# Kernel optimization log

Measured on AMD Instinct MI355X. Metric: run time of the kernel, lower is better.

Reference implementation:

```python
import jax, jax.numpy as jnp
import numpy as np

B, S, D, H = 4, 2048, 512, 8
DH = D // H


def setup_inputs() -> dict:
    key = jax.random.key(0)
    ks = jax.random.split(key, 6)
    embeddings = jax.random.normal(ks[0], (B, S, D), dtype=jnp.float32)
    token_masks = jax.random.randint(ks[1], (B, S), 0, 2, dtype=jnp.int32)
    # keras 'random_normal' initializer: stddev 0.05
    Wq = 0.05 * jax.random.normal(ks[2], (D, D), dtype=jnp.float32)
    Wk = 0.05 * jax.random.normal(ks[3], (D, D), dtype=jnp.float32)
    Wv = 0.05 * jax.random.normal(ks[4], (D, D), dtype=jnp.float32)
    Wo = 0.05 * jax.random.normal(ks[5], (D, D), dtype=jnp.float32)
    return {"embeddings": embeddings, "token_masks": token_masks,
            "Wq": Wq, "Wk": Wk, "Wv": Wv, "Wo": Wo}


def reference(embeddings, token_masks, Wq, Wk, Wv, Wo):
    b, s, d = embeddings.shape
    h, dh = H, d // H
    # QKV projections -> (b, h, s, dh)
    def split_heads(x):
        return x.reshape(b, s, h, dh).transpose(0, 2, 1, 3)
    Q = split_heads(embeddings @ Wq)
    K = split_heads(embeddings @ Wk)
    V = split_heads(embeddings @ Wv)
    scores = jnp.einsum('bhqd,bhkd->bhqk', Q, K) / jnp.sqrt(jnp.float32(dh))
    # causal (lower-triangular) mask combined with padding mask on both q and k
    causal = jnp.tril(jnp.ones((s, s), dtype=jnp.float32))
    tm = token_masks.astype(jnp.float32)
    attn_mask = causal[None, None, :, :] * tm[:, None, None, :] * tm[:, None, :, None]
    scores = jnp.where(attn_mask > 0, scores, jnp.float32(-1e30))
    weights = jax.nn.softmax(scores, axis=-1)  # dropout omitted (inference/eval mode)
    context = jnp.einsum('bhqk,bhkd->bhqd', weights, V)
    context = context.transpose(0, 2, 1, 3).reshape(b, s, d)
    return context @ Wo
```

## Files before the change

kernel.cpp:

```cpp
#include <hip/hip_runtime.h>
#include <hip/hip_bf16.h>
#include <stdint.h>

#define BATCH 4
#define SEQ 2048
#define DMODEL 512
#define NHEAD 8
#define HD 64

#define C1 0.18033688f
#define BIAS2 -23.0831207f

using f32x4 = __attribute__((ext_vector_type(4))) float;
using bfrag = __attribute__((ext_vector_type(8))) short;

__device__ __forceinline__ short f2bf(float f) {
  uint32_t x = __builtin_bit_cast(uint32_t, f);
  uint32_t r = (x + 0x7fffu + ((x >> 16) & 1u)) >> 16;
  return (short)r;
}
__device__ __forceinline__ short f2bf_fast(float f) {
  return (short)((__builtin_bit_cast(uint32_t, f) + 0x8000u) >> 16);
}
__device__ __forceinline__ float bf2f(short s) {
  return __builtin_bit_cast(float, ((uint32_t)(uint16_t)s) << 16);
}
__device__ __forceinline__ void gl_lds16(const void* g, void* l) {
  __builtin_amdgcn_global_load_lds(
      (const __attribute__((address_space(1))) void*)g,
      (__attribute__((address_space(3))) void*)l, 16, 0, 0);
}
__device__ __forceinline__ bool sniff_f32(const void* p, int tid) {
  const uint32_t* xw = (const uint32_t*)p;
  const int lane = tid & 63;
  const uint32_t w1 = xw[lane], w2 = xw[64 + lane];
  bool bad = (((w1 >> 7) & 0xffu) >= 0xB0u) | (((w1 >> 23) & 0xffu) >= 0xB0u) |
             (((w2 >> 7) & 0xffu) >= 0xB0u) | (((w2 >> 23) & 0xffu) >= 0xB0u);
  return __ballot(bad) != 0ull;
}

__global__ __launch_bounds__(256) void prep(const void* __restrict__ X,
                                            const void* __restrict__ w0,
                                            const void* __restrict__ w1,
                                            const void* __restrict__ w2,
                                            const void* __restrict__ w3,
                                            short* __restrict__ Xb,
                                            short* __restrict__ wtAll,
                                            float* __restrict__ mv) {
  const int blk = blockIdx.x, tid = threadIdx.x;
  if (blk < 2048) {
    const bool isf32 = sniff_f32(X, tid);
    const int i = (blk * 256 + tid) * 8;
    if (isf32) {
      const float* f = (const float*)X;
      short r[8];
#pragma unroll
      for (int j = 0; j < 8; ++j) r[j] = f2bf(f[i + j]);
      *(bfrag*)&Xb[i] = *(bfrag*)r;
    } else {
      *(bfrag*)&Xb[i] = *(const bfrag*)&((const short*)X)[i];
    }
  } else if (blk < 3072) {
    __shared__ short t[32][33];
    const int idx = blk - 2048;
    const int z = idx >> 8, rem = idx & 255;
    const void* in = (z == 0) ? w0 : (z == 1) ? w1 : (z == 2) ? w2 : w3;
    short* out = wtAll + (size_t)z * DMODEL * DMODEL;
    const int tx = tid & 31, ty = tid >> 5;
    const bool isf32 = sniff_f32(in, tid);
    const int n0 = (rem & 15) * 32, k0 = (rem >> 4) * 32;
#pragma unroll
    for (int i = ty; i < 32; i += 8) {
      const int idx2 = (k0 + i) * DMODEL + n0 + tx;
      t[i][tx] = isf32 ? f2bf(((const float*)in)[idx2]) : ((const short*)in)[idx2];
    }
    __syncthreads();
#pragma unroll
    for (int i = ty; i < 32; i += 8) out[(n0 + i) * DMODEL + k0 + tx] = t[tx][i];
  } else {
#pragma unroll
    for (int j = 0; j < 8; ++j) mv[tid * 8 + j] = 0.f;
  }
}

__global__ __launch_bounds__(256) void gemm_qkv(const short* __restrict__ X,
                                                const short* __restrict__ WtAll,
                                                short* __restrict__ Qo,
                                                short* __restrict__ Ko,
                                                short* __restrict__ Vo,
                                                float* __restrict__ mv) {
  __shared__ __align__(16) short As[128 * 32];
  __shared__ __align__(16) short Bs[128 * 32];
  const int which = blockIdx.z;
  const short* Wt = WtAll + which * DMODEL * DMODEL;
  const int m0 = blockIdx.y * 128, n0 = blockIdx.x * 128;
  const int tid = threadIdx.x, lane = tid & 63, wave = tid >> 6;
  const int l15 = lane & 15, quad = lane >> 4;
  const int wm = wave >> 1, wn = wave & 1;
  const int lrow = lane >> 2, lcol = (lane & 3) * 8;
  f32x4 acc[4][4] = {};
  for (int kc = 0; kc < DMODEL; kc += 32) {
#pragma unroll
    for (int i = 0; i < 2; ++i) {
      const int r0 = (wave * 2 + i) * 16;
      gl_lds16(&X[(size_t)(m0 + r0 + lrow) * DMODEL + kc + lcol], &As[r0 * 32]);
      gl_lds16(&Wt[(size_t)(n0 + r0 + lrow) * DMODEL + kc + lcol], &Bs[r0 * 32]);
    }
    __syncthreads();
    bfrag a[4], b[4];
#pragma unroll
    for (int t = 0; t < 4; ++t) {
      a[t] = *(const bfrag*)&As[(wm * 64 + t * 16 + l15) * 32 + quad * 8];
      b[t] = *(const bfrag*)&Bs[(wn * 64 + t * 16 + l15) * 32 + quad * 8];
    }
#pragma unroll
    for (int tm = 0; tm < 4; ++tm)
#pragma unroll
      for (int tn = 0; tn < 4; ++tn)
        acc[tm][tn] = __builtin_amdgcn_mfma_f32_16x16x32_bf16(a[tm], b[tn], acc[tm][tn], 0, 0, 0);
    __syncthreads();
  }
  short* O = (which == 0) ? Qo : (which == 1) ? Ko : Vo;
#pragma unroll
  for (int tn = 0; tn < 4; ++tn) {
    const int col = n0 + wn * 64 + tn * 16 + l15;
    const int h = col >> 6, d = col & 63;
#pragma unroll
    for (int tm = 0; tm < 4; ++tm) {
#pragma unroll
      for (int r = 0; r < 4; ++r) {
        const int row = m0 + wm * 64 + tm * 16 + quad * 4 + r;
        const int b = row >> 11, s = row & 2047;
        O[((b * NHEAD + h) * SEQ + s) * HD + d] = f2bf(acc[tm][tn][r]);
      }
    }
  }
  if (which == 2) {
    const int b = (m0 + wm * 64) >> 11;
#pragma unroll
    for (int tn = 0; tn < 4; ++tn) {
      float s = 0.f;
#pragma unroll
      for (int tm = 0; tm < 4; ++tm)
#pragma unroll
        for (int r = 0; r < 4; ++r) s += acc[tm][tn][r];
      s += __shfl_xor(s, 16);
      s += __shfl_xor(s, 32);
      if (quad == 0) {
        const int col = n0 + wn * 64 + tn * 16 + l15;
        const int h = col >> 6, d = col & 63;
        atomicAdd(&mv[(b * NHEAD + h) * 64 + d], s);
      }
    }
  }
}

__global__ __launch_bounds__(256) void gemm_out(const short* __restrict__ X,
                                                const short* __restrict__ Wt,
                                                float* __restrict__ O) {
  __shared__ __align__(16) short As[128 * 32];
  __shared__ __align__(16) short Bs[128 * 32];
  const int m0 = blockIdx.y * 128, n0 = blockIdx.x * 128;
  const int tid = threadIdx.x, lane = tid & 63, wave = tid >> 6;
  const int l15 = lane & 15, quad = lane >> 4;
  const int wm = wave >> 1, wn = wave & 1;
  const int lrow = lane >> 2, lcol = (lane & 3) * 8;
  f32x4 acc[4][4] = {};
  for (int kc = 0; kc < DMODEL; kc += 32) {
#pragma unroll
    for (int i = 0; i < 2; ++i) {
      const int r0 = (wave * 2 + i) * 16;
      gl_lds16(&X[(size_t)(m0 + r0 + lrow) * DMODEL + kc + lcol], &As[r0 * 32]);
      gl_lds16(&Wt[(size_t)(n0 + r0 + lrow) * DMODEL + kc + lcol], &Bs[r0 * 32]);
    }
    __syncthreads();
    bfrag a[4], b[4];
#pragma unroll
    for (int t = 0; t < 4; ++t) {
      a[t] = *(const bfrag*)&As[(wm * 64 + t * 16 + l15) * 32 + quad * 8];
      b[t] = *(const bfrag*)&Bs[(wn * 64 + t * 16 + l15) * 32 + quad * 8];
    }
#pragma unroll
    for (int tm = 0; tm < 4; ++tm)
#pragma unroll
      for (int tn = 0; tn < 4; ++tn)
        acc[tm][tn] = __builtin_amdgcn_mfma_f32_16x16x32_bf16(a[tm], b[tn], acc[tm][tn], 0, 0, 0);
    __syncthreads();
  }
#pragma unroll
  for (int tm = 0; tm < 4; ++tm)
#pragma unroll
    for (int tn = 0; tn < 4; ++tn) {
      const int col = n0 + wn * 64 + tn * 16 + l15;
#pragma unroll
      for (int r = 0; r < 4; ++r) {
        const int row = m0 + wm * 64 + tm * 16 + quad * 4 + r;
        O[(size_t)row * DMODEL + col] = acc[tm][tn][r];
      }
    }
}

__global__ __launch_bounds__(256, 4) void attn(const short* __restrict__ Q,
                                               const short* __restrict__ K,
                                               const short* __restrict__ V,
                                               const int* __restrict__ tmask,
                                               const float* __restrict__ meanV,
                                               short* __restrict__ ctx) {
  __shared__ __align__(16) short Ks[64 * 72];
  __shared__ __align__(16) short Vts[64 * 64];
  __shared__ __align__(16) short Ps[4 * 16 * 64];
  __shared__ int tmq[64];
  __shared__ int tmk[64];
  const int m2 = blockIdx.x >> 3, a3 = blockIdx.x & 7;
  const int j2 = blockIdx.y >> 3, b3 = blockIdx.y & 7;
  const int quart = (m2 + j2) & 3;
  const int qi = quart * 8 + ((quart & 1) ? (7 - a3) : a3);
  const int bh = j2 * 8 + b3;
  const int b = bh >> 3, h = bh & 7;
  const int q0 = qi * 64;
  const int tid = threadIdx.x, lane = tid & 63, wave = tid >> 6;
  const int l15 = lane & 15, quad = lane >> 4;
  const size_t base = (size_t)bh * SEQ * HD;

  bfrag qa0 = *(const bfrag*)&Q[base + (size_t)(q0 + wave * 16 + l15) * HD + quad * 8];
  bfrag qa1 = *(const bfrag*)&Q[base + (size_t)(q0 + wave * 16 + l15) * HD + 32 + quad * 8];
  if (tid < 64) tmq[tid] = tmask[b * SEQ + q0 + tid];

  f32x4 accO[4] = {};
  float lrow[4] = {0.f, 0.f, 0.f, 0.f};

  const int rp = tid >> 3, sgp = tid & 7;
  bfrag kA, kB, vA, vB;
  int tmreg = 0;

  auto prefetch = [&](int kc) {
    const size_t o0 = base + (size_t)(kc + 2 * rp) * HD + sgp * 8;
    kA = *(const bfrag*)&K[o0];
    kB = *(const bfrag*)&K[o0 + HD];
    vA = *(const bfrag*)&V[o0];
    vB = *(const bfrag*)&V[o0 + HD];
    if (tid < 64) tmreg = tmask[b * SEQ + kc + tid];
  };
  auto store_lds = [&]() {
    *(bfrag*)&Ks[(2 * rp) * 72 + sgp * 8] = kA;
    *(bfrag*)&Ks[(2 * rp + 1) * 72 + sgp * 8] = kB;
    const int g = ((rp >> 2) ^ ((sgp & 1) << 2) ^ (sgp >> 1)) & 7;
    const int kpos = (2 * rp) & 7;
#pragma unroll
    for (int j = 0; j < 8; ++j) {
      const uint32_t w = (uint32_t)(uint16_t)vA[j] | ((uint32_t)(uint16_t)vB[j] << 16);
      *(uint32_t*)&Vts[(sgp * 8 + j) * 64 + g * 8 + kpos] = w;
    }
    if (tid < 64) tmk[tid] = tmreg;
  };
  auto compute = [&](bool diag) {
    f32x4 sacc[4] = {};
#pragma unroll
    for (int t = 0; t < 4; ++t) {
      bfrag b0 = *(const bfrag*)&Ks[(t * 16 + l15) * 72 + quad * 8];
      sacc[t] = __builtin_amdgcn_mfma_f32_16x16x32_bf16(qa0, b0, sacc[t], 0, 0, 0);
    }
#pragma unroll
    for (int t = 0; t < 4; ++t) {
      bfrag b1 = *(const bfrag*)&Ks[(t * 16 + l15) * 72 + 32 + quad * 8];
      sacc[t] = __builtin_amdgcn_mfma_f32_16x16x32_bf16(qa1, b1, sacc[t], 0, 0, 0);
    }
    float badd[4];
#pragma unroll
    for (int t = 0; t < 4; ++t) badd[t] = tmk[t * 16 + l15] ? BIAS2 : -1e30f;
#pragma unroll
    for (int r = 0; r < 4; ++r) {
      const int m = quad * 4 + r;
#pragma unroll
      for (int t = 0; t < 4; ++t) {
        float p = exp2f(fmaf(sacc[t][r], C1, badd[t]));
        if (diag && (t * 16 + l15 > wave * 16 + m)) p = 0.f;
        lrow[r] += p;
        const int g = ((t * 2 + (l15 >> 3)) ^ (m & 7) ^ ((m >> 3) << 1)) & 7;
        Ps[wave * 1024 + m * 64 + g * 8 + (l15 & 7)] = f2bf_fast(p);
      }
    }
#pragma unroll
    for (int ks = 0; ks < 2; ++ks) {
#pragma unroll
      for (int t = 0; t < 4; ++t) {
        const int gp = ((ks * 4 + quad) ^ (l15 & 7) ^ ((l15 >> 3) << 1)) & 7;
        bfrag pa = *(const bfrag*)&Ps[wave * 1024 + l15 * 64 + gp * 8];
        const int d = t * 16 + l15;
        const int gv = ((ks * 4 + quad) ^ ((l15 >> 3) << 2) ^ t) & 7;
        bfrag vb = *(const bfrag*)&Vts[d * 64 + gv * 8];
        accO[t] = __builtin_amdgcn_mfma_f32_16x16x32_bf16(pa, vb, accO[t], 0, 0, 0);
      }
    }
  };

  prefetch(0);
  for (int kc = 0; kc <= q0; kc += 64) {
    __syncthreads();
    store_lds();
    __syncthreads();
    if (kc < q0) prefetch(kc + 64);
    compute(kc == q0);
  }

#pragma unroll
  for (int r = 0; r < 4; ++r) {
    float l = lrow[r];
    l += __shfl_xor(l, 1);
    l += __shfl_xor(l, 2);
    l += __shfl_xor(l, 4);
    l += __shfl_xor(l, 8);
    lrow[r] = 1.f / l;
  }
  const int qrow_loc = wave * 16 + quad * 4;
#pragma unroll
  for (int t = 0; t < 4; ++t) {
    const int d = t * 16 + l15;
    const float mvd = meanV[bh * 64 + d] * (1.f / 2048.f);
#pragma unroll
    for (int r = 0; r < 4; ++r) {
      const int row = qrow_loc + r;
      float val = accO[t][r] * lrow[r];
      if (tmq[row] == 0) val = mvd;
      ctx[((size_t)(b * SEQ + q0 + row)) * DMODEL + h * HD + d] = f2bf(val);
    }
  }
}

extern "C" void kernel_launch(void* const* d_in, const int* in_sizes, int n_in,
                              void* d_out, int out_size, void* d_ws, size_t ws_size,
                              hipStream_t stream) {
  const void* X = d_in[0];
  const int* tmask = (const int*)d_in[1];
  const void* Wq = d_in[2];
  const void* Wk = d_in[3];
  const void* Wv = d_in[4];
  const void* Wo = d_in[5];
  float* out = (float*)d_out;
  char* ws = (char*)d_ws;

  const size_t WELEM = (size_t)DMODEL * DMODEL;
  const size_t TELEM = (size_t)BATCH * NHEAD * SEQ * HD;

  float* mv = (float*)(ws + 4096);
  short* wt = (short*)(ws + 4096 + 8192);
  short* Xb = (short*)(ws + 4096 + 8192 + 2097152);
  short* Qb = Xb + TELEM;
  short* Kb = Qb + TELEM;
  short* Vb = Kb + TELEM;
  short* Cb = Vb + TELEM;

  prep<<<3073, 256, 0, stream>>>(X, Wq, Wk, Wv, Wo, Xb, wt, mv);
  gemm_qkv<<<dim3(4, 64, 3), 256, 0, stream>>>(Xb, wt, Qb, Kb, Vb, mv);
  attn<<<dim3(32, 32), 256, 0, stream>>>(Qb, Kb, Vb, tmask, mv, Cb);
  gemm_out<<<dim3(4, 64), 256, 0, stream>>>(Cb, wt + 3 * WELEM, out);
}
```

Before: 172.8 us.

## Keep attention probabilities in registers via transposed QK and permlane swaps

```diff
diff --git a/kernel.cpp b/kernel.cpp
--- a/kernel.cpp
+++ b/kernel.cpp
@@ -13,14 +13,12 @@
 
 using f32x4 = __attribute__((ext_vector_type(4))) float;
 using bfrag = __attribute__((ext_vector_type(8))) short;
+using u32x4 = __attribute__((ext_vector_type(4))) unsigned int;
 
 __device__ __forceinline__ short f2bf(float f) {
   uint32_t x = __builtin_bit_cast(uint32_t, f);
   uint32_t r = (x + 0x7fffu + ((x >> 16) & 1u)) >> 16;
   return (short)r;
-}
-__device__ __forceinline__ short f2bf_fast(float f) {
-  return (short)((__builtin_bit_cast(uint32_t, f) + 0x8000u) >> 16);
 }
 __device__ __forceinline__ float bf2f(short s) {
   return __builtin_bit_cast(float, ((uint32_t)(uint16_t)s) << 16);
@@ -37,6 +35,17 @@
   bool bad = (((w1 >> 7) & 0xffu) >= 0xB0u) | (((w1 >> 23) & 0xffu) >= 0xB0u) |
              (((w2 >> 7) & 0xffu) >= 0xB0u) | (((w2 >> 23) & 0xffu) >= 0xB0u);
   return __ballot(bad) != 0ull;
+}
+__device__ __forceinline__ uint32_t cvtpk(float lo, float hi) {
+  uint32_t r;
+  asm("v_cvt_pk_bf16_f32 %0, %1, %2" : "=v"(r) : "v"(lo), "v"(hi));
+  return r;
+}
+__device__ __forceinline__ void pl32swap(uint32_t& a, uint32_t& b) {
+  asm("v_permlane32_swap_b32 %0, %1" : "+v"(a), "+v"(b));
+}
+__device__ __forceinline__ void pl16swap(uint32_t& a, uint32_t& b) {
+  asm("v_permlane16_swap_b32 %0, %1" : "+v"(a), "+v"(b));
 }
 
 __global__ __launch_bounds__(256) void prep(const void* __restrict__ X,
@@ -208,9 +217,7 @@
                                                short* __restrict__ ctx) {
   __shared__ __align__(16) short Ks[64 * 72];
   __shared__ __align__(16) short Vts[64 * 64];
-  __shared__ __align__(16) short Ps[4 * 16 * 64];
   __shared__ int tmq[64];
-  __shared__ int tmk[64];
   const int m2 = blockIdx.x >> 3, a3 = blockIdx.x & 7;
   const int j2 = blockIdx.y >> 3, b3 = blockIdx.y & 7;
   const int quart = (m2 + j2) & 3;
@@ -227,11 +234,12 @@
   if (tid < 64) tmq[tid] = tmask[b * SEQ + q0 + tid];
 
   f32x4 accO[4] = {};
-  float lrow[4] = {0.f, 0.f, 0.f, 0.f};
+  float lq = 0.f;
+  const int qrow_w = wave * 16 + l15;
 
   const int rp = tid >> 3, sgp = tid & 7;
   bfrag kA, kB, vA, vB;
-  int tmreg = 0;
+  uint64_t km_next = 0;
 
   auto prefetch = [&](int kc) {
     const size_t o0 = base + (size_t)(kc + 2 * rp) * HD + sgp * 8;
@@ -239,7 +247,8 @@
     kB = *(const bfrag*)&K[o0 + HD];
     vA = *(const bfrag*)&V[o0];
     vB = *(const bfrag*)&V[o0 + HD];
-    if (tid < 64) tmreg = tmask[b * SEQ + kc + tid];
+    const int mt = tmask[b * SEQ + kc + lane];
+    km_next = __ballot(mt != 0);
   };
   auto store_lds = [&]() {
     *(bfrag*)&Ks[(2 * rp) * 72 + sgp * 8] = kA;
@@ -251,45 +260,47 @@
       const uint32_t w = (uint32_t)(uint16_t)vA[j] | ((uint32_t)(uint16_t)vB[j] << 16);
       *(uint32_t*)&Vts[(sgp * 8 + j) * 64 + g * 8 + kpos] = w;
     }
-    if (tid < 64) tmk[tid] = tmreg;
   };
-  auto compute = [&](bool diag) {
+  auto compute = [&](bool diag, uint64_t km) {
     f32x4 sacc[4] = {};
 #pragma unroll
     for (int t = 0; t < 4; ++t) {
-      bfrag b0 = *(const bfrag*)&Ks[(t * 16 + l15) * 72 + quad * 8];
-      sacc[t] = __builtin_amdgcn_mfma_f32_16x16x32_bf16(qa0, b0, sacc[t], 0, 0, 0);
-    }
-#pragma unroll
-    for (int t = 0; t < 4; ++t) {
-      bfrag b1 = *(const bfrag*)&Ks[(t * 16 + l15) * 72 + 32 + quad * 8];
-      sacc[t] = __builtin_amdgcn_mfma_f32_16x16x32_bf16(qa1, b1, sacc[t], 0, 0, 0);
-    }
-    float badd[4];
-#pragma unroll
-    for (int t = 0; t < 4; ++t) badd[t] = tmk[t * 16 + l15] ? BIAS2 : -1e30f;
-#pragma unroll
-    for (int r = 0; r < 4; ++r) {
-      const int m = quad * 4 + r;
+      bfrag k0 = *(const bfrag*)&Ks[(t * 16 + l15) * 72 + quad * 8];
+      sacc[t] = __builtin_amdgcn_mfma_f32_16x16x32_bf16(k0, qa0, sacc[t], 0, 0, 0);
+      bfrag k1 = *(const bfrag*)&Ks[(t * 16 + l15) * 72 + 32 + quad * 8];
+      sacc[t] = __builtin_amdgcn_mfma_f32_16x16x32_bf16(k1, qa1, sacc[t], 0, 0, 0);
+    }
+#pragma unroll
+    for (int ks = 0; ks < 2; ++ks) {
+      uint32_t w[4];
+#pragma unroll
+      for (int hh = 0; hh < 2; ++hh) {
+        const int t = 2 * ks + hh;
+        float pr[4];
+#pragma unroll
+        for (int r = 0; r < 4; ++r) {
+          const int k = t * 16 + quad * 4 + r;
+          const float badd = ((km >> k) & 1ull) ? BIAS2 : -1e30f;
+          float pv = exp2f(fmaf(sacc[t][r], C1, badd));
+          if (diag && (k > qrow_w)) pv = 0.f;
+          lq += pv;
+          pr[r] = pv;
+        }
+        w[2 * hh] = cvtpk(pr[0], pr[1]);
+        w[2 * hh + 1] = cvtpk(pr[2], pr[3]);
+      }
+      pl32swap(w[0], w[2]);
+      pl16swap(w[0], w[2]);
+      pl32swap(w[1], w[3]);
+      pl16swap(w[1], w[3]);
+      u32x4 pw = {w[0], w[1], w[2], w[3]};
+      bfrag paf = __builtin_bit_cast(bfrag, pw);
 #pragma unroll
       for (int t = 0; t < 4; ++t) {
-        float p = exp2f(fmaf(sacc[t][r], C1, badd[t]));
-        if (diag && (t * 16 + l15 > wave * 16 + m)) p = 0.f;
-        lrow[r] += p;
-        const int g = ((t * 2 + (l15 >> 3)) ^ (m & 7) ^ ((m >> 3) << 1)) & 7;
-        Ps[wave * 1024 + m * 64 + g * 8 + (l15 & 7)] = f2bf_fast(p);
-      }
-    }
-#pragma unroll
-    for (int ks = 0; ks < 2; ++ks) {
-#pragma unroll
-      for (int t = 0; t < 4; ++t) {
-        const int gp = ((ks * 4 + quad) ^ (l15 & 7) ^ ((l15 >> 3) << 1)) & 7;
-        bfrag pa = *(const bfrag*)&Ps[wave * 1024 + l15 * 64 + gp * 8];
         const int d = t * 16 + l15;
         const int gv = ((ks * 4 + quad) ^ ((l15 >> 3) << 2) ^ t) & 7;
         bfrag vb = *(const bfrag*)&Vts[d * 64 + gv * 8];
-        accO[t] = __builtin_amdgcn_mfma_f32_16x16x32_bf16(pa, vb, accO[t], 0, 0, 0);
+        accO[t] = __builtin_amdgcn_mfma_f32_16x16x32_bf16(paf, vb, accO[t], 0, 0, 0);
       }
     }
   };
@@ -298,20 +309,18 @@
   for (int kc = 0; kc <= q0; kc += 64) {
     __syncthreads();
     store_lds();
+    const uint64_t km = km_next;
     __syncthreads();
     if (kc < q0) prefetch(kc + 64);
-    compute(kc == q0);
-  }
-
-#pragma unroll
-  for (int r = 0; r < 4; ++r) {
-    float l = lrow[r];
-    l += __shfl_xor(l, 1);
-    l += __shfl_xor(l, 2);
-    l += __shfl_xor(l, 4);
-    l += __shfl_xor(l, 8);
-    lrow[r] = 1.f / l;
-  }
+    compute(kc == q0, km);
+  }
+
+  lq += __shfl_xor(lq, 16);
+  lq += __shfl_xor(lq, 32);
+  float linv[4];
+#pragma unroll
+  for (int r = 0; r < 4; ++r) linv[r] = 1.f / __shfl(lq, quad * 4 + r, 64);
+
   const int qrow_loc = wave * 16 + quad * 4;
 #pragma unroll
   for (int t = 0; t < 4; ++t) {
@@ -320,7 +329,7 @@
 #pragma unroll
     for (int r = 0; r < 4; ++r) {
       const int row = qrow_loc + r;
-      float val = accO[t][r] * lrow[r];
+      float val = accO[t][r] * linv[r];
       if (tmq[row] == 0) val = mvd;
       ctx[((size_t)(b * SEQ + q0 + row)) * DMODEL + h * HD + d] = f2bf(val);
     }
```

Result: slower. 178.7 us (+3.4%).

## Load K fragments directly into registers and ballot the key mask

Applied to the files above, without the earlier changes.

```diff
diff --git a/kernel.cpp b/kernel.cpp
--- a/kernel.cpp
+++ b/kernel.cpp
@@ -206,11 +206,9 @@
                                                const int* __restrict__ tmask,
                                                const float* __restrict__ meanV,
                                                short* __restrict__ ctx) {
-  __shared__ __align__(16) short Ks[64 * 72];
   __shared__ __align__(16) short Vts[64 * 64];
   __shared__ __align__(16) short Ps[4 * 16 * 64];
   __shared__ int tmq[64];
-  __shared__ int tmk[64];
   const int m2 = blockIdx.x >> 3, a3 = blockIdx.x & 7;
   const int j2 = blockIdx.y >> 3, b3 = blockIdx.y & 7;
   const int quart = (m2 + j2) & 3;
@@ -230,20 +228,26 @@
   float lrow[4] = {0.f, 0.f, 0.f, 0.f};
 
   const int rp = tid >> 3, sgp = tid & 7;
-  bfrag kA, kB, vA, vB;
-  int tmreg = 0;
-
-  auto prefetch = [&](int kc) {
+  bfrag vA, vB;
+  bfrag kf0[4], kf1[4];
+  uint64_t km_next = 0;
+
+  auto prefetch_v = [&](int kc) {
     const size_t o0 = base + (size_t)(kc + 2 * rp) * HD + sgp * 8;
-    kA = *(const bfrag*)&K[o0];
-    kB = *(const bfrag*)&K[o0 + HD];
     vA = *(const bfrag*)&V[o0];
     vB = *(const bfrag*)&V[o0 + HD];
-    if (tid < 64) tmreg = tmask[b * SEQ + kc + tid];
+    const int mt = tmask[b * SEQ + kc + lane];
+    km_next = __ballot(mt != 0);
+  };
+  auto loadK = [&](int kc) {
+#pragma unroll
+    for (int t = 0; t < 4; ++t) {
+      const size_t ro = base + (size_t)(kc + t * 16 + l15) * HD + quad * 8;
+      kf0[t] = *(const bfrag*)&K[ro];
+      kf1[t] = *(const bfrag*)&K[ro + 32];
+    }
   };
   auto store_lds = [&]() {
-    *(bfrag*)&Ks[(2 * rp) * 72 + sgp * 8] = kA;
-    *(bfrag*)&Ks[(2 * rp + 1) * 72 + sgp * 8] = kB;
     const int g = ((rp >> 2) ^ ((sgp & 1) << 2) ^ (sgp >> 1)) & 7;
     const int kpos = (2 * rp) & 7;
 #pragma unroll
@@ -251,23 +255,19 @@
       const uint32_t w = (uint32_t)(uint16_t)vA[j] | ((uint32_t)(uint16_t)vB[j] << 16);
       *(uint32_t*)&Vts[(sgp * 8 + j) * 64 + g * 8 + kpos] = w;
     }
-    if (tid < 64) tmk[tid] = tmreg;
   };
-  auto compute = [&](bool diag) {
+  auto compute = [&](bool diag, uint64_t km, int kc) {
     f32x4 sacc[4] = {};
 #pragma unroll
     for (int t = 0; t < 4; ++t) {
-      bfrag b0 = *(const bfrag*)&Ks[(t * 16 + l15) * 72 + quad * 8];
-      sacc[t] = __builtin_amdgcn_mfma_f32_16x16x32_bf16(qa0, b0, sacc[t], 0, 0, 0);
-    }
-#pragma unroll
-    for (int t = 0; t < 4; ++t) {
-      bfrag b1 = *(const bfrag*)&Ks[(t * 16 + l15) * 72 + 32 + quad * 8];
-      sacc[t] = __builtin_amdgcn_mfma_f32_16x16x32_bf16(qa1, b1, sacc[t], 0, 0, 0);
-    }
+      sacc[t] = __builtin_amdgcn_mfma_f32_16x16x32_bf16(qa0, kf0[t], sacc[t], 0, 0, 0);
+      sacc[t] = __builtin_amdgcn_mfma_f32_16x16x32_bf16(qa1, kf1[t], sacc[t], 0, 0, 0);
+    }
+    if (kc < q0) loadK(kc + 64);
     float badd[4];
 #pragma unroll
-    for (int t = 0; t < 4; ++t) badd[t] = tmk[t * 16 + l15] ? BIAS2 : -1e30f;
+    for (int t = 0; t < 4; ++t)
+      badd[t] = ((km >> (t * 16 + l15)) & 1ull) ? BIAS2 : -1e30f;
 #pragma unroll
     for (int r = 0; r < 4; ++r) {
       const int m = quad * 4 + r;
@@ -294,13 +294,15 @@
     }
   };
 
-  prefetch(0);
+  prefetch_v(0);
+  loadK(0);
   for (int kc = 0; kc <= q0; kc += 64) {
     __syncthreads();
     store_lds();
-    __syncthreads();
-    if (kc < q0) prefetch(kc + 64);
-    compute(kc == q0);
+    const uint64_t km = km_next;
+    __syncthreads();
+    if (kc < q0) prefetch_v(kc + 64);
+    compute(kc == q0, km, kc);
   }
 
 #pragma unroll
```

New measurement: 230.6 us. +33.5%, slower.

## Balance causal attention work by split-K pairing of query tiles with combine kernel

Applied to the files above, without the earlier changes.

```diff
diff --git a/kernel.cpp b/kernel.cpp
--- a/kernel.cpp
+++ b/kernel.cpp
@@ -205,126 +205,182 @@
                                                const short* __restrict__ V,
                                                const int* __restrict__ tmask,
                                                const float* __restrict__ meanV,
-                                               short* __restrict__ ctx) {
+                                               short* __restrict__ ctx,
+                                               float* __restrict__ Pn0,
+                                               float* __restrict__ Pl0,
+                                               float* __restrict__ Pn1,
+                                               float* __restrict__ Pl1) {
   __shared__ __align__(16) short Ks[64 * 72];
   __shared__ __align__(16) short Vts[64 * 64];
   __shared__ __align__(16) short Ps[4 * 16 * 64];
-  __shared__ int tmq[64];
-  __shared__ int tmk[64];
-  const int m2 = blockIdx.x >> 3, a3 = blockIdx.x & 7;
-  const int j2 = blockIdx.y >> 3, b3 = blockIdx.y & 7;
-  const int quart = (m2 + j2) & 3;
-  const int qi = quart * 8 + ((quart & 1) ? (7 - a3) : a3);
-  const int bh = j2 * 8 + b3;
+  const int bh = blockIdx.x, j = blockIdx.y;
   const int b = bh >> 3, h = bh & 7;
-  const int q0 = qi * 64;
   const int tid = threadIdx.x, lane = tid & 63, wave = tid >> 6;
   const int l15 = lane & 15, quad = lane >> 4;
+  const int rp = tid >> 3, sgp = tid & 7;
   const size_t base = (size_t)bh * SEQ * HD;
 
-  bfrag qa0 = *(const bfrag*)&Q[base + (size_t)(q0 + wave * 16 + l15) * HD + quad * 8];
-  bfrag qa1 = *(const bfrag*)&Q[base + (size_t)(q0 + wave * 16 + l15) * HD + 32 + quad * 8];
-  if (tid < 64) tmq[tid] = tmask[b * SEQ + q0 + tid];
-
-  f32x4 accO[4] = {};
-  float lrow[4] = {0.f, 0.f, 0.f, 0.f};
-
-  const int rp = tid >> 3, sgp = tid & 7;
-  bfrag kA, kB, vA, vB;
-  int tmreg = 0;
-
-  auto prefetch = [&](int kc) {
-    const size_t o0 = base + (size_t)(kc + 2 * rp) * HD + sgp * 8;
-    kA = *(const bfrag*)&K[o0];
-    kB = *(const bfrag*)&K[o0 + HD];
-    vA = *(const bfrag*)&V[o0];
-    vB = *(const bfrag*)&V[o0 + HD];
-    if (tid < 64) tmreg = tmask[b * SEQ + kc + tid];
+  auto run_phase = [&](int q0, int kc0, int nch, bool dg, bool direct,
+                       float* pn, float* pl) {
+    bfrag qa0 = *(const bfrag*)&Q[base + (size_t)(q0 + wave * 16 + l15) * HD + quad * 8];
+    bfrag qa1 = *(const bfrag*)&Q[base + (size_t)(q0 + wave * 16 + l15) * HD + 32 + quad * 8];
+    f32x4 accO[4] = {};
+    float lrow[4] = {0.f, 0.f, 0.f, 0.f};
+    bfrag kA, kB, vA, vB;
+    uint64_t km_next = 0;
+
+    auto prefetch = [&](int kc) {
+      const size_t o0 = base + (size_t)(kc + 2 * rp) * HD + sgp * 8;
+      kA = *(const bfrag*)&K[o0];
+      kB = *(const bfrag*)&K[o0 + HD];
+      vA = *(const bfrag*)&V[o0];
+      vB = *(const bfrag*)&V[o0 + HD];
+      km_next = __ballot(tmask[b * SEQ + kc + lane] != 0);
+    };
+    auto store_lds = [&]() {
+      *(bfrag*)&Ks[(2 * rp) * 72 + sgp * 8] = kA;
+      *(bfrag*)&Ks[(2 * rp + 1) * 72 + sgp * 8] = kB;
+      const int g = ((rp >> 2) ^ ((sgp & 1) << 2) ^ (sgp >> 1)) & 7;
+      const int kpos = (2 * rp) & 7;
+#pragma unroll
+      for (int jj = 0; jj < 8; ++jj) {
+        const uint32_t w = (uint32_t)(uint16_t)vA[jj] | ((uint32_t)(uint16_t)vB[jj] << 16);
+        *(uint32_t*)&Vts[(sgp * 8 + jj) * 64 + g * 8 + kpos] = w;
+      }
+    };
+    auto compute = [&](bool diag, uint64_t km) {
+      f32x4 sacc[4] = {};
+#pragma unroll
+      for (int t = 0; t < 4; ++t) {
+        bfrag b0 = *(const bfrag*)&Ks[(t * 16 + l15) * 72 + quad * 8];
+        sacc[t] = __builtin_amdgcn_mfma_f32_16x16x32_bf16(qa0, b0, sacc[t], 0, 0, 0);
+      }
+#pragma unroll
+      for (int t = 0; t < 4; ++t) {
+        bfrag b1 = *(const bfrag*)&Ks[(t * 16 + l15) * 72 + 32 + quad * 8];
+        sacc[t] = __builtin_amdgcn_mfma_f32_16x16x32_bf16(qa1, b1, sacc[t], 0, 0, 0);
+      }
+      float badd[4];
+#pragma unroll
+      for (int t = 0; t < 4; ++t)
+        badd[t] = ((km >> (t * 16 + l15)) & 1ull) ? BIAS2 : -1e30f;
+#pragma unroll
+      for (int r = 0; r < 4; ++r) {
+        const int m = quad * 4 + r;
+#pragma unroll
+        for (int t = 0; t < 4; ++t) {
+          float p = exp2f(fmaf(sacc[t][r], C1, badd[t]));
+          if (diag && (t * 16 + l15 > wave * 16 + m)) p = 0.f;
+          lrow[r] += p;
+          const int g = ((t * 2 + (l15 >> 3)) ^ (m & 7) ^ ((m >> 3) << 1)) & 7;
+          Ps[wave * 1024 + m * 64 + g * 8 + (l15 & 7)] = f2bf_fast(p);
+        }
+      }
+#pragma unroll
+      for (int ks = 0; ks < 2; ++ks) {
+#pragma unroll
+        for (int t = 0; t < 4; ++t) {
+          const int gp = ((ks * 4 + quad) ^ (l15 & 7) ^ ((l15 >> 3) << 1)) & 7;
+          bfrag pa = *(const bfrag*)&Ps[wave * 1024 + l15 * 64 + gp * 8];
+          const int d = t * 16 + l15;
+          const int gv = ((ks * 4 + quad) ^ ((l15 >> 3) << 2) ^ t) & 7;
+          bfrag vb = *(const bfrag*)&Vts[d * 64 + gv * 8];
+          accO[t] = __builtin_amdgcn_mfma_f32_16x16x32_bf16(pa, vb, accO[t], 0, 0, 0);
+        }
+      }
+    };
+
+    prefetch(kc0);
+    for (int c = 0; c < nch; ++c) {
+      const int kc = kc0 + c * 64;
+      __syncthreads();
+      store_lds();
+      const uint64_t km = km_next;
+      __syncthreads();
+      if (c + 1 < nch) prefetch(kc + 64);
+      compute(dg && (c == nch - 1), km);
+    }
+
+#pragma unroll
+    for (int r = 0; r < 4; ++r) {
+      float l = lrow[r];
+      l += __shfl_xor(l, 1);
+      l += __shfl_xor(l, 2);
+      l += __shfl_xor(l, 4);
+      l += __shfl_xor(l, 8);
+      lrow[r] = l;
+    }
+    const int qrow_loc = wave * 16 + quad * 4;
+    if (direct) {
+      const uint64_t qm = __ballot(tmask[b * SEQ + q0 + lane] != 0);
+      float inv[4];
+#pragma unroll
+      for (int r = 0; r < 4; ++r) inv[r] = 1.f / lrow[r];
+#pragma unroll
+      for (int t = 0; t < 4; ++t) {
+        const int d = t * 16 + l15;
+        const float mvd = meanV[bh * 64 + d] * (1.f / 2048.f);
+#pragma unroll
+        for (int r = 0; r < 4; ++r) {
+          const int row = qrow_loc + r;
+          float val = accO[t][r] * inv[r];
+          if (!((qm >> row) & 1ull)) val = mvd;
+          ctx[((size_t)(b * SEQ + q0 + row)) * DMODEL + h * HD + d] = f2bf(val);
+        }
+      }
+    } else {
+#pragma unroll
+      for (int t = 0; t < 4; ++t)
+#pragma unroll
+        for (int r = 0; r < 4; ++r)
+          pn[(qrow_loc + r) * 64 + t * 16 + l15] = accO[t][r];
+      if (l15 == 0) {
+#pragma unroll
+        for (int r = 0; r < 4; ++r) pl[qrow_loc + r] = lrow[r];
+      }
+    }
   };
-  auto store_lds = [&]() {
-    *(bfrag*)&Ks[(2 * rp) * 72 + sgp * 8] = kA;
-    *(bfrag*)&Ks[(2 * rp + 1) * 72 + sgp * 8] = kB;
-    const int g = ((rp >> 2) ^ ((sgp & 1) << 2) ^ (sgp >> 1)) & 7;
-    const int kpos = (2 * rp) & 7;
-#pragma unroll
-    for (int j = 0; j < 8; ++j) {
-      const uint32_t w = (uint32_t)(uint16_t)vA[j] | ((uint32_t)(uint16_t)vB[j] << 16);
-      *(uint32_t*)&Vts[(sgp * 8 + j) * 64 + g * 8 + kpos] = w;
-    }
-    if (tid < 64) tmk[tid] = tmreg;
-  };
-  auto compute = [&](bool diag) {
-    f32x4 sacc[4] = {};
-#pragma unroll
-    for (int t = 0; t < 4; ++t) {
-      bfrag b0 = *(const bfrag*)&Ks[(t * 16 + l15) * 72 + quad * 8];
-      sacc[t] = __builtin_amdgcn_mfma_f32_16x16x32_bf16(qa0, b0, sacc[t], 0, 0, 0);
-    }
-#pragma unroll
-    for (int t = 0; t < 4; ++t) {
-      bfrag b1 = *(const bfrag*)&Ks[(t * 16 + l15) * 72 + 32 + quad * 8];
-      sacc[t] = __builtin_amdgcn_mfma_f32_16x16x32_bf16(qa1, b1, sacc[t], 0, 0, 0);
-    }
-    float badd[4];
-#pragma unroll
-    for (int t = 0; t < 4; ++t) badd[t] = tmk[t * 16 + l15] ? BIAS2 : -1e30f;
-#pragma unroll
-    for (int r = 0; r < 4; ++r) {
-      const int m = quad * 4 + r;
-#pragma unroll
-      for (int t = 0; t < 4; ++t) {
-        float p = exp2f(fmaf(sacc[t][r], C1, badd[t]));
-        if (diag && (t * 16 + l15 > wave * 16 + m)) p = 0.f;
-        lrow[r] += p;
-        const int g = ((t * 2 + (l15 >> 3)) ^ (m & 7) ^ ((m >> 3) << 1)) & 7;
-        Ps[wave * 1024 + m * 64 + g * 8 + (l15 & 7)] = f2bf_fast(p);
-      }
-    }
-#pragma unroll
-    for (int ks = 0; ks < 2; ++ks) {
-#pragma unroll
-      for (int t = 0; t < 4; ++t) {
-        const int gp = ((ks * 4 + quad) ^ (l15 & 7) ^ ((l15 >> 3) << 1)) & 7;
-        bfrag pa = *(const bfrag*)&Ps[wave * 1024 + l15 * 64 + gp * 8];
-        const int d = t * 16 + l15;
-        const int gv = ((ks * 4 + quad) ^ ((l15 >> 3) << 2) ^ t) & 7;
-        bfrag vb = *(const bfrag*)&Vts[d * 64 + gv * 8];
-        accO[t] = __builtin_amdgcn_mfma_f32_16x16x32_bf16(pa, vb, accO[t], 0, 0, 0);
-      }
-    }
-  };
-
-  prefetch(0);
-  for (int kc = 0; kc <= q0; kc += 64) {
-    __syncthreads();
-    store_lds();
-    __syncthreads();
-    if (kc < q0) prefetch(kc + 64);
-    compute(kc == q0);
-  }
-
-#pragma unroll
-  for (int r = 0; r < 4; ++r) {
-    float l = lrow[r];
-    l += __shfl_xor(l, 1);
-    l += __shfl_xor(l, 2);
-    l += __shfl_xor(l, 4);
-    l += __shfl_xor(l, 8);
-    lrow[r] = 1.f / l;
-  }
-  const int qrow_loc = wave * 16 + quad * 4;
-#pragma unroll
-  for (int t = 0; t < 4; ++t) {
-    const int d = t * 16 + l15;
-    const float mvd = meanV[bh * 64 + d] * (1.f / 2048.f);
-#pragma unroll
-    for (int r = 0; r < 4; ++r) {
-      const int row = qrow_loc + r;
-      float val = accO[t][r] * lrow[r];
-      if (tmq[row] == 0) val = mvd;
-      ctx[((size_t)(b * SEQ + q0 + row)) * DMODEL + h * HD + d] = f2bf(val);
-    }
-  }
+
+  if (j < 16) {
+    run_phase(64 * j, 0, j + 1, true, true, nullptr, nullptr);
+    const int tl = 15 - j;
+    run_phase(64 * (31 - j), 1024, 16 - j, true, false,
+              Pn1 + (size_t)(bh * 16 + tl) * 4096, Pl1 + (bh * 16 + tl) * 64);
+  } else {
+    run_phase(64 * j, 0, 16, false, false,
+              Pn0 + (size_t)(bh * 16 + (j - 16)) * 4096,
+              Pl0 + (bh * 16 + (j - 16)) * 64);
+  }
+}
+
+__global__ __launch_bounds__(256) void combine(const float* __restrict__ Pn0,
+                                               const float* __restrict__ Pl0,
+                                               const float* __restrict__ Pn1,
+                                               const float* __restrict__ Pl1,
+                                               const int* __restrict__ tmask,
+                                               const float* __restrict__ meanV,
+                                               short* __restrict__ ctx) {
+  const int tile = blockIdx.x;
+  const int bh = tile >> 4, t = tile & 15;
+  const int b = bh >> 3, h = bh & 7;
+  const int q0 = (16 + t) * 64;
+  const int tid = threadIdx.x;
+  const int row = tid >> 2, c0 = (tid & 3) * 16;
+  const float l = Pl0[tile * 64 + row] + Pl1[tile * 64 + row];
+  const int tq = tmask[b * SEQ + q0 + row];
+  const float inv = tq ? 1.f / l : 0.f;
+  const float* n0 = Pn0 + (size_t)tile * 4096 + row * 64 + c0;
+  const float* n1 = Pn1 + (size_t)tile * 4096 + row * 64 + c0;
+  short out[16];
+#pragma unroll
+  for (int i = 0; i < 16; ++i) {
+    float v = tq ? (n0[i] + n1[i]) * inv
+                 : meanV[bh * 64 + c0 + i] * (1.f / 2048.f);
+    out[i] = f2bf(v);
+  }
+  short* dst = &ctx[((size_t)(b * SEQ + q0 + row)) * DMODEL + h * HD + c0];
+  *(bfrag*)dst = *(bfrag*)out;
+  *(bfrag*)(dst + 8) = *(bfrag*)(out + 8);
 }
 
 extern "C" void kernel_launch(void* const* d_in, const int* in_sizes, int n_in,
@@ -349,9 +405,15 @@
   short* Kb = Qb + TELEM;
   short* Vb = Kb + TELEM;
   short* Cb = Vb + TELEM;
+  float* Pn0 = (float*)Xb;
+  float* Pn1 = (float*)(Cb + TELEM);
+  float* Pl0 = Pn1 + (size_t)512 * 4096;
+  float* Pl1 = Pl0 + 512 * 64;
 
   prep<<<3073, 256, 0, stream>>>(X, Wq, Wk, Wv, Wo, Xb, wt, mv);
   gemm_qkv<<<dim3(4, 64, 3), 256, 0, stream>>>(Xb, wt, Qb, Kb, Vb, mv);
-  attn<<<dim3(32, 32), 256, 0, stream>>>(Qb, Kb, Vb, tmask, mv, Cb);
+  attn<<<dim3(32, 32), 256, 0, stream>>>(Qb, Kb, Vb, tmask, mv, Cb,
+                                         Pn0, Pl0, Pn1, Pl1);
+  combine<<<512, 256, 0, stream>>>(Pn0, Pl0, Pn1, Pl1, tmask, mv, Cb);
   gemm_out<<<dim3(4, 64), 256, 0, stream>>>(Cb, wt + 3 * WELEM, out);
 }
```

Result: slower. 182.2 us (+5.4%).
